# Performance work log

Measured on AMD Instinct MI355X. Metric: run time of the kernel, lower is better.

Reference implementation:

```python
import jax, jax.numpy as jnp
import numpy as np

BANDS = [2,3,3,3,3,3,3,3,3,3,3,8,8,8,8,8,8,8,8,8,8,8,8,16,16,16,16,16,16,16,17]
CHANNELS = 128
MAX_C = 34  # 2 * max(band)
EPS = 1e-5


def setup_inputs() -> dict:
    key = jax.random.key(0)
    ks = jax.random.split(key, 5)
    B, F, T = 16, 257, 1000
    x = jax.random.normal(ks[0], (B, F, T, 2), dtype=jnp.float32)
    gn_w = jax.random.normal(ks[1], (len(BANDS), MAX_C), dtype=jnp.float32)
    gn_b = jax.random.normal(ks[2], (len(BANDS), MAX_C), dtype=jnp.float32)
    fc_w = jax.random.normal(ks[3], (len(BANDS), CHANNELS, MAX_C), dtype=jnp.float32) * 0.05
    fc_b = jax.random.normal(ks[4], (len(BANDS), CHANNELS), dtype=jnp.float32) * 0.05
    return {"x": x, "gn_w": gn_w, "gn_b": gn_b, "fc_w": fc_w, "fc_b": fc_b}


def reference(x, gn_w, gn_b, fc_w, fc_b):
    # x: [B, F=257, T, 2]. torch forward transposes to [B, T, F, 2] then slices freq;
    # equivalent here: slice freq on dim 1, then move time forward.
    B, F, T, _ = x.shape
    outs = []
    f0 = 0
    for i, b in enumerate(BANDS):
        c = 2 * b
        # [B, b, T, 2] -> [B, T, b, 2] -> [B, T, 2b]
        xb = jnp.transpose(x[:, f0:f0 + b], (0, 2, 1, 3)).reshape(B, T, c)
        # GroupNorm(1, c) on [B, c, T]: normalize over (c, T) per sample
        mu = jnp.mean(xb, axis=(1, 2), keepdims=True)
        var = jnp.var(xb, axis=(1, 2), keepdims=True)
        xn = (xb - mu) * jax.lax.rsqrt(var + EPS)
        xn = xn * gn_w[i, :c] + gn_b[i, :c]
        # Linear(c -> CHANNELS)
        out = jnp.einsum('btc,oc->bto', xn, fc_w[i, :, :c]) + fc_b[i]
        outs.append(out)
        f0 += b
    # z: [B, T, CHANNELS, n_bands]
    return jnp.stack(outs, axis=3)
```

## Files before the change

### kernel.cpp

```cpp
#include <hip/hip_runtime.h>
#include <hip/hip_bf16.h>


typedef short short8 __attribute__((ext_vector_type(8)));
typedef float floatx4 __attribute__((ext_vector_type(4)));

__device__ __forceinline__ unsigned short f2bf(float f) {
  unsigned int u = __float_as_uint(f);
  u = (u + 0x7fffu + ((u >> 16) & 1u)) >> 16;
  return (unsigned short)u;
}

__device__ __forceinline__ int band_of_f(int f) {
  if (f < 2) return 0;
  if (f < 32) return 1 + (f - 2) / 3;
  if (f < 128) return 11 + (f - 32) / 8;
  if (f < 240) return 23 + (f - 128) / 16;
  return 30;
}
__device__ __forceinline__ int f0_of_band(int i) {
  if (i == 0) return 0;
  if (i <= 10) return 2 + 3 * (i - 1);
  if (i <= 22) return 32 + 8 * (i - 11);
  if (i <= 29) return 128 + 16 * (i - 23);
  return 240;
}
__device__ __forceinline__ int c_of_band(int i) {
  if (i == 0) return 4;
  if (i <= 10) return 6;
  if (i <= 22) return 16;
  if (i <= 29) return 32;
  return 34;
}
__device__ __forceinline__ int bw_of_band(int i) {
  if (i == 0) return 2;
  if (i <= 10) return 3;
  if (i <= 22) return 8;
  if (i <= 29) return 16;
  return 17;
}

__global__ __launch_bounds__(256) void prep_kernel(
    const float* __restrict__ x,
    const float* __restrict__ gn_w,
    const float* __restrict__ gn_b,
    const float* __restrict__ fc_w,
    float* __restrict__ sA, float* __restrict__ sB,
    unsigned short* __restrict__ wf) {
  const int blk = blockIdx.x;
  const int tid = threadIdx.x;
  __shared__ float redS[4], redQ[4];
  __shared__ float musig[2];

  if (blk >= 496) {
    const int gid = (blk - 496) * 256 + tid;
    const int ks = gid >> 9;
    const int rem = gid & 511;
    const int ot = rem >> 6;
    const int l = rem & 63;
    const int o = ot * 16 + (l & 15);
    const int kbase = ks * 32 + ((l >> 4) << 3);
    short8 v;
#pragma unroll
    for (int j = 0; j < 8; ++j) {
      int kp = kbase + j;
      int i = (kp >= 960) ? 30 : (kp >> 5);
      int cidx = kp - (i << 5);
      int c = c_of_band(i);
      unsigned short w =
          (cidx < c) ? f2bf(fc_w[(i * 128 + o) * 34 + cidx]) : (unsigned short)0;
      v[j] = (short)w;
    }
    ((short8*)wf)[gid] = v;
    return;
  }

  const int i = blk % 31;
  const int b = blk / 31;
  const int bw = bw_of_band(i);
  const int f0 = f0_of_band(i);
  const long start = ((long)(b * 257 + f0)) * 2000;
  const float4* p4 = (const float4*)(x + start);
  const int nchunk = bw * 500;

  float s = 0.f, sq = 0.f;
  int e = tid;
  for (; e + 768 < nchunk; e += 1024) {
    float4 w0 = p4[e];
    float4 w1 = p4[e + 256];
    float4 w2 = p4[e + 512];
    float4 w3 = p4[e + 768];
    s += (w0.x + w0.y + w0.z + w0.w) + (w1.x + w1.y + w1.z + w1.w) +
         (w2.x + w2.y + w2.z + w2.w) + (w3.x + w3.y + w3.z + w3.w);
    sq += (w0.x * w0.x + w0.y * w0.y + w0.z * w0.z + w0.w * w0.w) +
          (w1.x * w1.x + w1.y * w1.y + w1.z * w1.z + w1.w * w1.w) +
          (w2.x * w2.x + w2.y * w2.y + w2.z * w2.z + w2.w * w2.w) +
          (w3.x * w3.x + w3.y * w3.y + w3.z * w3.z + w3.w * w3.w);
  }
  for (; e < nchunk; e += 256) {
    float4 v = p4[e];
    s += v.x + v.y + v.z + v.w;
    sq += v.x * v.x + v.y * v.y + v.z * v.z + v.w * v.w;
  }
#pragma unroll
  for (int off = 32; off > 0; off >>= 1) {
    s += __shfl_down(s, off);
    sq += __shfl_down(sq, off);
  }
  if ((tid & 63) == 0) { redS[tid >> 6] = s; redQ[tid >> 6] = sq; }
  __syncthreads();
  if (tid == 0) {
    float S = redS[0] + redS[1] + redS[2] + redS[3];
    float Q = redQ[0] + redQ[1] + redQ[2] + redQ[3];
    float cnt = (float)(bw * 2000);
    float mu = S / cnt;
    float var = Q / cnt - mu * mu;
    musig[0] = mu;
    musig[1] = rsqrtf(var + 1e-5f);
  }
  __syncthreads();
  const int c = c_of_band(i);
  if (tid < c) {
    float mu = musig[0], rs = musig[1];
    float gw = gn_w[i * 34 + tid];
    float gb = gn_b[i * 34 + tid];
    float a = rs * gw;
    int kp = i * 32 + tid;
    sA[(b << 10) + kp] = a;
    sB[(b << 10) + kp] = gb - mu * a;
  }
}

__global__ __launch_bounds__(256, 4) void main_kernel(
    const float* __restrict__ x,
    const float* __restrict__ sA, const float* __restrict__ sB,
    const unsigned short* __restrict__ wf,
    const float* __restrict__ fc_b,
    float* __restrict__ out) {
  const int tc = blockIdx.x;
  const int q = blockIdx.y;
  const int b = blockIdx.z;
  const int t0 = tc * 16;
  if (t0 >= 1000) return;
  const int tid = threadIdx.x;

  __shared__ __align__(16) unsigned char lds_raw[16 * 1032 * 2];
  unsigned short(*xn)[1032] = (unsigned short(*)[1032])lds_raw;
  float(*stage)[496] = (float(*)[496])lds_raw;

  const int wv = tid >> 6;
  const int l = tid & 63;
  const int quad = l >> 4;
  const int n = l & 15;

  float bias[8][2];
#pragma unroll
  for (int it = 0; it < 8; ++it) {
    const int band = wv + it * 4;
    if (band >= 31) break;
#pragma unroll
    for (int ot = 0; ot < 2; ++ot)
      bias[it][ot] = fc_b[band * 128 + (((q << 1) | ot) << 4) + n];
  }

  for (int e = tid; e < 2064; e += 256)
    ((uint4*)lds_raw)[e] = make_uint4(0u, 0u, 0u, 0u);
  __syncthreads();

  const float4* xq = (const float4*)(x + (long)b * 514000 + (long)t0 * 2);
  const float* sAb = sA + (b << 10);
  const float* sBb = sB + (b << 10);
#pragma unroll
  for (int half = 0; half < 2; ++half) {
    float4 xv[4];
    float2 av[4], sv[4];
    int row[4], kps[4];
    bool val[4];
#pragma unroll
    for (int j = 0; j < 4; ++j) {
      int d = tid + (half * 4 + j) * 256;
      int f = d >> 3;
      int kpair = d & 7;
      int i = band_of_f(f);
      int kp = (i << 5) + 2 * (f - f0_of_band(i));
      bool v = (t0 + 2 * kpair < 1000);
      row[j] = 2 * kpair; kps[j] = kp; val[j] = v;
      if (v) {
        xv[j] = xq[f * 500 + kpair];
        av[j] = *(const float2*)(sAb + kp);
        sv[j] = *(const float2*)(sBb + kp);
      }
    }
#pragma unroll
    for (int j = 0; j < 4; ++j) {
      if (val[j]) {
        unsigned int r0 = f2bf(xv[j].x * av[j].x + sv[j].x);
        unsigned int r1 = f2bf(xv[j].y * av[j].y + sv[j].y);
        unsigned int r2 = f2bf(xv[j].z * av[j].x + sv[j].x);
        unsigned int r3 = f2bf(xv[j].w * av[j].y + sv[j].y);
        *(unsigned int*)&xn[row[j]][kps[j]] = r0 | (r1 << 16);
        *(unsigned int*)&xn[row[j] + 1][kps[j]] = r2 | (r3 << 16);
      }
    }
  }
  if (tid < 8 && t0 + 2 * tid < 1000) {
    float4 v = xq[256 * 500 + tid];
    float2 av = *(const float2*)(sAb + 992);
    float2 sv = *(const float2*)(sBb + 992);
    unsigned int r0 = f2bf(v.x * av.x + sv.x);
    unsigned int r1 = f2bf(v.y * av.y + sv.y);
    unsigned int r2 = f2bf(v.z * av.x + sv.x);
    unsigned int r3 = f2bf(v.w * av.y + sv.y);
    *(unsigned int*)&xn[2 * tid][992] = r0 | (r1 << 16);
    *(unsigned int*)&xn[2 * tid + 1][992] = r2 | (r3 << 16);
  }
  __syncthreads();

  floatx4 acc[8][2];
#pragma unroll
  for (int it = 0; it < 8; ++it) {
    const int band = wv + it * 4;
    if (band >= 31) break;
    const bool dbl = (band == 30);
    short8 a0 = *(const short8*)&xn[n][(band << 5) + (quad << 3)];
#pragma unroll
    for (int ot = 0; ot < 2; ++ot) {
      const int OT = (q << 1) | ot;
      float bv = bias[it][ot];
      floatx4 a = {bv, bv, bv, bv};
      short8 b0 = ((const short8*)wf)[(band * 8 + OT) * 64 + l];
      a = __builtin_amdgcn_mfma_f32_16x16x32_bf16(a0, b0, a, 0, 0, 0);
      if (dbl) {
        short8 a1 = *(const short8*)&xn[n][992 + (quad << 3)];
        short8 b1 = ((const short8*)wf)[(31 * 8 + OT) * 64 + l];
        a = __builtin_amdgcn_mfma_f32_16x16x32_bf16(a1, b1, a, 0, 0, 0);
      }
      acc[it][ot] = a;
    }
  }
  __syncthreads();

#pragma unroll
  for (int ot = 0; ot < 2; ++ot) {
    if (ot) __syncthreads();
#pragma unroll
    for (int it = 0; it < 8; ++it) {
      const int band = wv + it * 4;
      if (band >= 31) break;
#pragma unroll
      for (int r = 0; r < 4; ++r)
        stage[(quad << 2) + r][n * 31 + band] = acc[it][ot][r];
    }
    __syncthreads();
    for (int e = tid; e < 16 * 124; e += 256) {
      int m = e / 124;
      int d = e - m * 124;
      int t = t0 + m;
      if (t < 1000) {
        uint4 v = ((const uint4*)&stage[m][0])[d];
        ((uint4*)out)[(long)(b * 1000 + t) * 992 + q * 248 + ot * 124 + d] = v;
      }
    }
  }
}

extern "C" void kernel_launch(void* const* d_in, const int* in_sizes, int n_in,
                              void* d_out, int out_size, void* d_ws, size_t ws_size,
                              hipStream_t stream) {
  const float* x = (const float*)d_in[0];
  const float* gn_w = (const float*)d_in[1];
  const float* gn_b = (const float*)d_in[2];
  const float* fc_w = (const float*)d_in[3];
  const float* fc_b = (const float*)d_in[4];
  float* out = (float*)d_out;

  float* sA = (float*)d_ws;
  float* sB = sA + 16 * 1024;
  unsigned short* wf = (unsigned short*)(sB + 16 * 1024);

  prep_kernel<<<560, 256, 0, stream>>>(x, gn_w, gn_b, fc_w, sA, sB, wf);
  main_kernel<<<dim3(64, 4, 16), 256, 0, stream>>>(x, sA, sB, wf, fc_b, out);
}
```

Baseline: 317.4 us.

## Split normalization into separate kernel writing bf16 tiles to workspace

Moves the normalize-and-convert-to-bf16 step out of the main GEMM kernel into its own kernel. That kernel writes padded bf16 tiles to workspace, so each tile is built once per (batch, time chunk) rather than four times, once per output quarter. The main kernel then copies the prebuilt tile into LDS. The trade-off is an extra kernel launch plus a workspace round trip of about 33 MB, and the original fused path is kept as a fallback when the workspace is too small.

New measurement: 326.8 us. +2.9%, slower.

```diff
diff --git a/kernel.cpp b/kernel.cpp
--- a/kernel.cpp
+++ b/kernel.cpp
@@ -131,37 +131,17 @@
   }
 }
 
-__global__ __launch_bounds__(256, 4) void main_kernel(
+__global__ __launch_bounds__(256, 4) void norm_kernel(
     const float* __restrict__ x,
     const float* __restrict__ sA, const float* __restrict__ sB,
-    const unsigned short* __restrict__ wf,
-    const float* __restrict__ fc_b,
-    float* __restrict__ out) {
+    unsigned short* __restrict__ xnG) {
   const int tc = blockIdx.x;
-  const int q = blockIdx.y;
-  const int b = blockIdx.z;
+  const int b = blockIdx.y;
   const int t0 = tc * 16;
-  if (t0 >= 1000) return;
   const int tid = threadIdx.x;
 
   __shared__ __align__(16) unsigned char lds_raw[16 * 1032 * 2];
   unsigned short(*xn)[1032] = (unsigned short(*)[1032])lds_raw;
-  float(*stage)[496] = (float(*)[496])lds_raw;
-
-  const int wv = tid >> 6;
-  const int l = tid & 63;
-  const int quad = l >> 4;
-  const int n = l & 15;
-
-  float bias[8][2];
-#pragma unroll
-  for (int it = 0; it < 8; ++it) {
-    const int band = wv + it * 4;
-    if (band >= 31) break;
-#pragma unroll
-    for (int ot = 0; ot < 2; ++ot)
-      bias[it][ot] = fc_b[band * 128 + (((q << 1) | ot) << 4) + n];
-  }
 
   for (int e = tid; e < 2064; e += 256)
     ((uint4*)lds_raw)[e] = make_uint4(0u, 0u, 0u, 0u);
@@ -216,6 +196,55 @@
   }
   __syncthreads();
 
+  uint4* dst = (uint4*)(xnG + (long)(b * 63 + tc) * 16512);
+#pragma unroll
+  for (int k = 0; k < 8; ++k)
+    dst[tid + k * 256] = ((const uint4*)lds_raw)[tid + k * 256];
+  if (tid < 16) dst[2048 + tid] = ((const uint4*)lds_raw)[2048 + tid];
+}
+
+__global__ __launch_bounds__(256, 4) void main_kernel(
+    const unsigned short* __restrict__ xnG,
+    const unsigned short* __restrict__ wf,
+    const float* __restrict__ fc_b,
+    float* __restrict__ out) {
+  const int tc = blockIdx.x;
+  const int q = blockIdx.y;
+  const int b = blockIdx.z;
+  const int t0 = tc * 16;
+  if (t0 >= 1000) return;
+  const int tid = threadIdx.x;
+
+  __shared__ __align__(16) unsigned char lds_raw[16 * 1032 * 2];
+  unsigned short(*xn)[1032] = (unsigned short(*)[1032])lds_raw;
+  float(*stage)[496] = (float(*)[496])lds_raw;
+
+  const int wv = tid >> 6;
+  const int l = tid & 63;
+  const int quad = l >> 4;
+  const int n = l & 15;
+
+  float bias[8][2];
+#pragma unroll
+  for (int it = 0; it < 8; ++it) {
+    const int band = wv + it * 4;
+    if (band >= 31) break;
+#pragma unroll
+    for (int ot = 0; ot < 2; ++ot)
+      bias[it][ot] = fc_b[band * 128 + (((q << 1) | ot) << 4) + n];
+  }
+
+  const uint4* src = (const uint4*)(xnG + (long)(b * 63 + tc) * 16512);
+  uint4 tmp[8];
+#pragma unroll
+  for (int k = 0; k < 8; ++k) tmp[k] = src[tid + k * 256];
+  uint4 tail;
+  if (tid < 16) tail = src[2048 + tid];
+#pragma unroll
+  for (int k = 0; k < 8; ++k) ((uint4*)lds_raw)[tid + k * 256] = tmp[k];
+  if (tid < 16) ((uint4*)lds_raw)[2048 + tid] = tail;
+  __syncthreads();
+
   floatx4 acc[8][2];
 #pragma unroll
   for (int it = 0; it < 8; ++it) {
@@ -264,6 +293,139 @@
   }
 }
 
+__global__ __launch_bounds__(256, 4) void main_kernel_fb(
+    const float* __restrict__ x,
+    const float* __restrict__ sA, const float* __restrict__ sB,
+    const unsigned short* __restrict__ wf,
+    const float* __restrict__ fc_b,
+    float* __restrict__ out) {
+  const int tc = blockIdx.x;
+  const int q = blockIdx.y;
+  const int b = blockIdx.z;
+  const int t0 = tc * 16;
+  if (t0 >= 1000) return;
+  const int tid = threadIdx.x;
+
+  __shared__ __align__(16) unsigned char lds_raw[16 * 1032 * 2];
+  unsigned short(*xn)[1032] = (unsigned short(*)[1032])lds_raw;
+  float(*stage)[496] = (float(*)[496])lds_raw;
+
+  const int wv = tid >> 6;
+  const int l = tid & 63;
+  const int quad = l >> 4;
+  const int n = l & 15;
+
+  float bias[8][2];
+#pragma unroll
+  for (int it = 0; it < 8; ++it) {
+    const int band = wv + it * 4;
+    if (band >= 31) break;
+#pragma unroll
+    for (int ot = 0; ot < 2; ++ot)
+      bias[it][ot] = fc_b[band * 128 + (((q << 1) | ot) << 4) + n];
+  }
+
+  for (int e = tid; e < 2064; e += 256)
+    ((uint4*)lds_raw)[e] = make_uint4(0u, 0u, 0u, 0u);
+  __syncthreads();
+
+  const float4* xq = (const float4*)(x + (long)b * 514000 + (long)t0 * 2);
+  const float* sAb = sA + (b << 10);
+  const float* sBb = sB + (b << 10);
+#pragma unroll
+  for (int half = 0; half < 2; ++half) {
+    float4 xv[4];
+    float2 av[4], sv[4];
+    int row[4], kps[4];
+    bool val[4];
+#pragma unroll
+    for (int j = 0; j < 4; ++j) {
+      int d = tid + (half * 4 + j) * 256;
+      int f = d >> 3;
+      int kpair = d & 7;
+      int i = band_of_f(f);
+      int kp = (i << 5) + 2 * (f - f0_of_band(i));
+      bool v = (t0 + 2 * kpair < 1000);
+      row[j] = 2 * kpair; kps[j] = kp; val[j] = v;
+      if (v) {
+        xv[j] = xq[f * 500 + kpair];
+        av[j] = *(const float2*)(sAb + kp);
+        sv[j] = *(const float2*)(sBb + kp);
+      }
+    }
+#pragma unroll
+    for (int j = 0; j < 4; ++j) {
+      if (val[j]) {
+        unsigned int r0 = f2bf(xv[j].x * av[j].x + sv[j].x);
+        unsigned int r1 = f2bf(xv[j].y * av[j].y + sv[j].y);
+        unsigned int r2 = f2bf(xv[j].z * av[j].x + sv[j].x);
+        unsigned int r3 = f2bf(xv[j].w * av[j].y + sv[j].y);
+        *(unsigned int*)&xn[row[j]][kps[j]] = r0 | (r1 << 16);
+        *(unsigned int*)&xn[row[j] + 1][kps[j]] = r2 | (r3 << 16);
+      }
+    }
+  }
+  if (tid < 8 && t0 + 2 * tid < 1000) {
+    float4 v = xq[256 * 500 + tid];
+    float2 av = *(const float2*)(sAb + 992);
+    float2 sv = *(const float2*)(sBb + 992);
+    unsigned int r0 = f2bf(v.x * av.x + sv.x);
+    unsigned int r1 = f2bf(v.y * av.y + sv.y);
+    unsigned int r2 = f2bf(v.z * av.x + sv.x);
+    unsigned int r3 = f2bf(v.w * av.y + sv.y);
+    *(unsigned int*)&xn[2 * tid][992] = r0 | (r1 << 16);
+    *(unsigned int*)&xn[2 * tid + 1][992] = r2 | (r3 << 16);
+  }
+  __syncthreads();
+
+  floatx4 acc[8][2];
+#pragma unroll
+  for (int it = 0; it < 8; ++it) {
+    const int band = wv + it * 4;
+    if (band >= 31) break;
+    const bool dbl = (band == 30);
+    short8 a0 = *(const short8*)&xn[n][(band << 5) + (quad << 3)];
+#pragma unroll
+    for (int ot = 0; ot < 2; ++ot) {
+      const int OT = (q << 1) | ot;
+      float bv = bias[it][ot];
+      floatx4 a = {bv, bv, bv, bv};
+      short8 b0 = ((const short8*)wf)[(band * 8 + OT) * 64 + l];
+      a = __builtin_amdgcn_mfma_f32_16x16x32_bf16(a0, b0, a, 0, 0, 0);
+      if (dbl) {
+        short8 a1 = *(const short8*)&xn[n][992 + (quad << 3)];
+        short8 b1 = ((const short8*)wf)[(31 * 8 + OT) * 64 + l];
+        a = __builtin_amdgcn_mfma_f32_16x16x32_bf16(a1, b1, a, 0, 0, 0);
+      }
+      acc[it][ot] = a;
+    }
+  }
+  __syncthreads();
+
+#pragma unroll
+  for (int ot = 0; ot < 2; ++ot) {
+    if (ot) __syncthreads();
+#pragma unroll
+    for (int it = 0; it < 8; ++it) {
+      const int band = wv + it * 4;
+      if (band >= 31) break;
+#pragma unroll
+      for (int r = 0; r < 4; ++r)
+        stage[(quad << 2) + r][n * 31 + band] = acc[it][ot][r];
+    }
+    __syncthreads();
+    for (int e = tid; e < 16 * 124; e += 256) {
+      int m = e / 124;
+      int d = e - m * 124;
+      int t = t0 + m;
+      if (t < 1000) {
+        uint4 v = ((const uint4*)&stage[m][0])[d];
+        ((uint4*)out)[(long)(b * 1000 + t) * 992 + q * 248 + ot * 124 + d] = v;
+      }
+    }
+  }
+}
+
 extern "C" void kernel_launch(void* const* d_in, const int* in_sizes, int n_in,
                               void* d_out, int out_size, void* d_ws, size_t ws_size,
                               hipStream_t stream) {
@@ -277,7 +439,14 @@
   float* sA = (float*)d_ws;
   float* sB = sA + 16 * 1024;
   unsigned short* wf = (unsigned short*)(sB + 16 * 1024);
+  unsigned short* xnG = (unsigned short*)((char*)d_ws + 393216);
+  const size_t need = 393216 + (size_t)1008 * 16512 * 2;
 
   prep_kernel<<<560, 256, 0, stream>>>(x, gn_w, gn_b, fc_w, sA, sB, wf);
-  main_kernel<<<dim3(64, 4, 16), 256, 0, stream>>>(x, sA, sB, wf, fc_b, out);
-}
+  if (ws_size >= need) {
+    norm_kernel<<<dim3(63, 16), 256, 0, stream>>>(x, sA, sB, xnG);
+    main_kernel<<<dim3(64, 4, 16), 256, 0, stream>>>(xnG, wf, fc_b, out);
+  } else {
+    main_kernel_fb<<<dim3(64, 4, 16), 256, 0, stream>>>(x, sA, sB, wf, fc_b, out);
+  }
+}
```

## Halve output-channel grid split and interleave GroupNorm scale/shift into one float4

Applied to the files above, without the earlier changes.

Each block now computes 4 output-channel tiles instead of 2, so the grid's y dimension drops from 4 to 2. This halves the redundant loading and normalisation of the x tile into LDS across blocks. The per-channel scale and shift are interleaved so one float4 load replaces two float2 loads. Accumulator registers double, and launch bounds drop to 3 blocks per SM, which may lower occupancy and overlap.

Measured after the change: 317.3 us. About the same (-0.0%).

```diff
diff --git a/kernel.cpp b/kernel.cpp
--- a/kernel.cpp
+++ b/kernel.cpp
@@ -45,7 +45,7 @@
     const float* __restrict__ gn_w,
     const float* __restrict__ gn_b,
     const float* __restrict__ fc_w,
-    float* __restrict__ sA, float* __restrict__ sB,
+    float* __restrict__ sAB,
     unsigned short* __restrict__ wf) {
   const int blk = blockIdx.x;
   const int tid = threadIdx.x;
@@ -126,19 +126,19 @@
     float gb = gn_b[i * 34 + tid];
     float a = rs * gw;
     int kp = i * 32 + tid;
-    sA[(b << 10) + kp] = a;
-    sB[(b << 10) + kp] = gb - mu * a;
-  }
-}
-
-__global__ __launch_bounds__(256, 4) void main_kernel(
+    sAB[(b << 11) + ((kp >> 1) << 2) + (kp & 1)] = a;
+    sAB[(b << 11) + ((kp >> 1) << 2) + 2 + (kp & 1)] = gb - mu * a;
+  }
+}
+
+__global__ __launch_bounds__(256, 3) void main_kernel(
     const float* __restrict__ x,
-    const float* __restrict__ sA, const float* __restrict__ sB,
+    const float* __restrict__ sAB,
     const unsigned short* __restrict__ wf,
     const float* __restrict__ fc_b,
     float* __restrict__ out) {
   const int tc = blockIdx.x;
-  const int q = blockIdx.y;
+  const int qh = blockIdx.y;
   const int b = blockIdx.z;
   const int t0 = tc * 16;
   if (t0 >= 1000) return;
@@ -153,14 +153,14 @@
   const int quad = l >> 4;
   const int n = l & 15;
 
-  float bias[8][2];
+  float bias[8][4];
 #pragma unroll
   for (int it = 0; it < 8; ++it) {
     const int band = wv + it * 4;
     if (band >= 31) break;
 #pragma unroll
-    for (int ot = 0; ot < 2; ++ot)
-      bias[it][ot] = fc_b[band * 128 + (((q << 1) | ot) << 4) + n];
+    for (int p = 0; p < 4; ++p)
+      bias[it][p] = fc_b[band * 128 + (((qh << 2) | p) << 4) + n];
   }
 
   for (int e = tid; e < 2064; e += 256)
@@ -168,12 +168,10 @@
   __syncthreads();
 
   const float4* xq = (const float4*)(x + (long)b * 514000 + (long)t0 * 2);
-  const float* sAb = sA + (b << 10);
-  const float* sBb = sB + (b << 10);
+  const float4* sq = (const float4*)(sAB + (b << 11));
 #pragma unroll
   for (int half = 0; half < 2; ++half) {
-    float4 xv[4];
-    float2 av[4], sv[4];
+    float4 xv[4], ab[4];
     int row[4], kps[4];
     bool val[4];
 #pragma unroll
@@ -187,17 +185,16 @@
       row[j] = 2 * kpair; kps[j] = kp; val[j] = v;
       if (v) {
         xv[j] = xq[f * 500 + kpair];
-        av[j] = *(const float2*)(sAb + kp);
-        sv[j] = *(const float2*)(sBb + kp);
+        ab[j] = sq[kp >> 1];
       }
     }
 #pragma unroll
     for (int j = 0; j < 4; ++j) {
       if (val[j]) {
-        unsigned int r0 = f2bf(xv[j].x * av[j].x + sv[j].x);
-        unsigned int r1 = f2bf(xv[j].y * av[j].y + sv[j].y);
-        unsigned int r2 = f2bf(xv[j].z * av[j].x + sv[j].x);
-        unsigned int r3 = f2bf(xv[j].w * av[j].y + sv[j].y);
+        unsigned int r0 = f2bf(xv[j].x * ab[j].x + ab[j].z);
+        unsigned int r1 = f2bf(xv[j].y * ab[j].y + ab[j].w);
+        unsigned int r2 = f2bf(xv[j].z * ab[j].x + ab[j].z);
+        unsigned int r3 = f2bf(xv[j].w * ab[j].y + ab[j].w);
         *(unsigned int*)&xn[row[j]][kps[j]] = r0 | (r1 << 16);
         *(unsigned int*)&xn[row[j] + 1][kps[j]] = r2 | (r3 << 16);
       }
@@ -205,18 +202,17 @@
   }
   if (tid < 8 && t0 + 2 * tid < 1000) {
     float4 v = xq[256 * 500 + tid];
-    float2 av = *(const float2*)(sAb + 992);
-    float2 sv = *(const float2*)(sBb + 992);
-    unsigned int r0 = f2bf(v.x * av.x + sv.x);
-    unsigned int r1 = f2bf(v.y * av.y + sv.y);
-    unsigned int r2 = f2bf(v.z * av.x + sv.x);
-    unsigned int r3 = f2bf(v.w * av.y + sv.y);
+    float4 ab = sq[496];
+    unsigned int r0 = f2bf(v.x * ab.x + ab.z);
+    unsigned int r1 = f2bf(v.y * ab.y + ab.w);
+    unsigned int r2 = f2bf(v.z * ab.x + ab.z);
+    unsigned int r3 = f2bf(v.w * ab.y + ab.w);
     *(unsigned int*)&xn[2 * tid][992] = r0 | (r1 << 16);
     *(unsigned int*)&xn[2 * tid + 1][992] = r2 | (r3 << 16);
   }
   __syncthreads();
 
-  floatx4 acc[8][2];
+  floatx4 acc[8][4];
 #pragma unroll
   for (int it = 0; it < 8; ++it) {
     const int band = wv + it * 4;
@@ -224,9 +220,9 @@
     const bool dbl = (band == 30);
     short8 a0 = *(const short8*)&xn[n][(band << 5) + (quad << 3)];
 #pragma unroll
-    for (int ot = 0; ot < 2; ++ot) {
-      const int OT = (q << 1) | ot;
-      float bv = bias[it][ot];
+    for (int p = 0; p < 4; ++p) {
+      const int OT = (qh << 2) | p;
+      float bv = bias[it][p];
       floatx4 a = {bv, bv, bv, bv};
       short8 b0 = ((const short8*)wf)[(band * 8 + OT) * 64 + l];
       a = __builtin_amdgcn_mfma_f32_16x16x32_bf16(a0, b0, a, 0, 0, 0);
@@ -235,30 +231,31 @@
         short8 b1 = ((const short8*)wf)[(31 * 8 + OT) * 64 + l];
         a = __builtin_amdgcn_mfma_f32_16x16x32_bf16(a1, b1, a, 0, 0, 0);
       }
-      acc[it][ot] = a;
-    }
-  }
-  __syncthreads();
-
-#pragma unroll
-  for (int ot = 0; ot < 2; ++ot) {
-    if (ot) __syncthreads();
+      acc[it][p] = a;
+    }
+  }
+  __syncthreads();
+
+#pragma unroll
+  for (int p = 0; p < 4; ++p) {
+    if (p) __syncthreads();
 #pragma unroll
     for (int it = 0; it < 8; ++it) {
       const int band = wv + it * 4;
       if (band >= 31) break;
 #pragma unroll
       for (int r = 0; r < 4; ++r)
-        stage[(quad << 2) + r][n * 31 + band] = acc[it][ot][r];
+        stage[(quad << 2) + r][n * 31 + band] = acc[it][p][r];
     }
     __syncthreads();
+    const int OT = (qh << 2) | p;
     for (int e = tid; e < 16 * 124; e += 256) {
       int m = e / 124;
       int d = e - m * 124;
       int t = t0 + m;
       if (t < 1000) {
         uint4 v = ((const uint4*)&stage[m][0])[d];
-        ((uint4*)out)[(long)(b * 1000 + t) * 992 + q * 248 + ot * 124 + d] = v;
+        ((uint4*)out)[(long)(b * 1000 + t) * 992 + OT * 124 + d] = v;
       }
     }
   }
@@ -274,10 +271,9 @@
   const float* fc_b = (const float*)d_in[4];
   float* out = (float*)d_out;
 
-  float* sA = (float*)d_ws;
-  float* sB = sA + 16 * 1024;
-  unsigned short* wf = (unsigned short*)(sB + 16 * 1024);
-
-  prep_kernel<<<560, 256, 0, stream>>>(x, gn_w, gn_b, fc_w, sA, sB, wf);
-  main_kernel<<<dim3(64, 4, 16), 256, 0, stream>>>(x, sA, sB, wf, fc_b, out);
-}
+  float* sAB = (float*)d_ws;
+  unsigned short* wf = (unsigned short*)(sAB + 16 * 2048);
+
+  prep_kernel<<<560, 256, 0, stream>>>(x, gn_w, gn_b, fc_w, sAB, wf);
+  main_kernel<<<dim3(64, 2, 16), 256, 0, stream>>>(x, sAB, wf, fc_b, out);
+}
```
